# Optimization experiments

Hardware: AMD Instinct MI355X
Metric: run time of the kernel (lower is better)

Reference implementation:

```python
import jax, jax.numpy as jnp
import numpy as np

BIG = 1e8  # sentinel 'infinite' squared distance (sqrt(BIG) >> max real distance)


def _edt_sq(feat):
    """Exact squared Euclidean distance transform to the nearest True pixel.
    feat: (H, W) bool. Separable 1-D min-plus envelopes (exact, matches
    scipy.ndimage.distance_transform_edt with unit sampling)."""
    H, W = feat.shape
    f = jnp.where(feat, 0.0, BIG).astype(jnp.float32)
    iw = jnp.arange(W, dtype=jnp.float32)
    sqw = (iw[:, None] - iw[None, :]) ** 2                      # (Wx, Wy)
    d1 = jnp.min(f[:, None, :] + sqw[None, :, :], axis=-1)      # (H, W) row pass
    ih = jnp.arange(H, dtype=jnp.float32)
    sqh = (ih[:, None] - ih[None, :]) ** 2                      # (Hx, Hy)
    d2 = jnp.min(d1[None, :, :] + sqh[:, :, None], axis=1)      # (H, W) col pass
    return d2


def _phi_one(mask):
    # pos: distance to nearest mask==1 pixel (scipy edt of 1-mask)
    # neg: distance to nearest mask==0 pixel (scipy edt of mask)
    pos = jnp.sqrt(_edt_sq(mask))
    neg = jnp.sqrt(_edt_sq(~mask))
    s = mask.sum()
    return jnp.where(s == 0, pos,
                     jnp.where(s == mask.size, -neg, pos - neg + 1.0))


def _boundary_loss(logits, targets):
    B, C, H, W = logits.shape
    probs = jax.nn.softmax(logits, axis=1)
    # one-hot scatter: (B,H,W) -> (B,C,H,W)
    oh = jax.nn.one_hot(targets, C, dtype=jnp.float32).transpose(0, 3, 1, 2)
    masks = (oh > 0.5).reshape(B * C, H, W)
    phi = jax.lax.map(_phi_one, masks).reshape(B, C, H, W)
    phi = jax.lax.stop_gradient(phi)  # torch computes phi under no_grad
    return jnp.mean(probs * phi)


def setup_inputs() -> dict:
    key = jax.random.key(0)
    k1, k2 = jax.random.split(key)
    B, C, H, W = 8, 4, 384, 384
    logits = jax.random.normal(k1, (B, C, H, W), dtype=jnp.float32)
    targets = jax.random.randint(k2, (B, H, W), 0, C, dtype=jnp.int32)
    return {"logits": logits, "targets": targets}


def reference(logits, targets):
    return _boundary_loss(logits, targets)
```

## Files before the change

kernel.cpp:

```cpp
#include <hip/hip_runtime.h>


#define BB 8
#define CC 4
#define HH 384
#define WW 384
#define HW (HH * WW)
#define EDT16_BYTES ((size_t)BB * CC * HW * 2)
#define NTOT 4718592.0f

__global__ __launch_bounds__(384) void k_rowedt(const int* __restrict__ targets,
                                                unsigned short* __restrict__ edt16,
                                                float* __restrict__ out) {
    const int blk = blockIdx.x;
    const int b = blk / HH;
    const int i = blk - b * HH;
    const int j = threadIdx.x;
    const int wv = j >> 6, ln = j & 63;

    __shared__ unsigned long long msk[CC][6];
    const int tj = targets[((size_t)b * HH + i) * WW + j];

    #pragma unroll
    for (int c = 0; c < CC; ++c) {
        const unsigned long long m = __ballot(tj == c);
        if (ln == 0) msk[c][wv] = m;
    }
    __syncthreads();

    #pragma unroll
    for (int c = 0; c < CC; ++c) {
        const unsigned long long w = msk[c][wv];
        int dR = 0xFFFF;
        const unsigned long long x = (ln == 63) ? 0ull : (w >> (ln + 1));
        if (x) {
            dR = __builtin_ctzll(x) + 1;
        } else {
            for (int k = wv + 1; k < 6; ++k) {
                const unsigned long long wk = msk[c][k];
                if (wk) { dR = 64 * k + __builtin_ctzll(wk) - j; break; }
            }
        }
        int dL = 0xFFFF;
        const unsigned long long y = (ln == 0) ? 0ull : (w << (64 - ln));
        if (y) {
            dL = __builtin_clzll(y) + 1;
        } else {
            for (int k = wv - 1; k >= 0; --k) {
                const unsigned long long wk = msk[c][k];
                if (wk) { dL = j - (64 * k + 63 - __builtin_clzll(wk)); break; }
            }
        }
        const int fd = (tj == c) ? 0 : (dR < dL ? dR : dL);
        edt16[(size_t)(b * CC + c) * HW + (size_t)i * WW + j] = (unsigned short)fd;
    }

    if (blk == 0 && j == 0) out[0] = 0.0f;
}

__global__ __launch_bounds__(384) void k_coledt(const unsigned short* __restrict__ edt16,
                                                float* __restrict__ phi) {
    const int blk = blockIdx.x;
    const int b = blk >> 5;
    const int tile = blk & 31;
    const int j0 = tile * 12;
    const int col = threadIdx.x % 12;
    const int rg  = threadIdx.x / 12;

    __shared__ unsigned short dls[CC][HH][13];

    #pragma unroll
    for (int c = 0; c < CC; ++c) {
        #pragma unroll
        for (int k = 0; k < 12; ++k) {
            const int i = rg * 12 + k;
            dls[c][i][col] =
                edt16[(size_t)(b * CC + c) * HW + (size_t)i * WW + j0 + col];
        }
    }
    __syncthreads();

    #pragma unroll 1
    for (int k = 0; k < 12; ++k) {
        const int i = rg * 12 + k;
        float r4[CC];
        #pragma unroll
        for (int c = 0; c < CC; ++c) {
            const unsigned int v0 = dls[c][i][col];
            float best = (float)(v0 * v0);
            float dd = 1.0f, odd = 3.0f;
            int lo = i, hi = i;
            while (dd < best) {
                lo = (lo > 0) ? lo - 1 : 0;
                hi = (hi < HH - 1) ? hi + 1 : HH - 1;
                const unsigned int a = dls[c][lo][col];
                const unsigned int e = dls[c][hi][col];
                const float ca = (float)(a * a) + dd;
                const float cb = (float)(e * e) + dd;
                best = fminf(best, fminf(ca, cb));
                dd += odd; odd += 2.0f;
            }
            r4[c] = sqrtf(best);
        }
        const float n0 = fminf(r4[1], fminf(r4[2], r4[3]));
        const float n1 = fminf(r4[0], fminf(r4[2], r4[3]));
        const float n2 = fminf(r4[0], fminf(r4[1], r4[3]));
        const float n3 = fminf(r4[0], fminf(r4[1], r4[2]));
        const size_t po = (size_t)i * WW + j0 + col;
        const size_t pb = (size_t)b * CC * HW;
        phi[pb + 0 * HW + po] = r4[0] - n0 + 1.0f;
        phi[pb + 1 * HW + po] = r4[1] - n1 + 1.0f;
        phi[pb + 2 * HW + po] = r4[2] - n2 + 1.0f;
        phi[pb + 3 * HW + po] = r4[3] - n3 + 1.0f;
    }
}

__global__ __launch_bounds__(256) void k_loss(const float* __restrict__ logits,
                                              const float* __restrict__ phi,
                                              float* __restrict__ out) {
    const int tid = blockIdx.x * 256 + threadIdx.x;
    const int b = tid / (HW / 4);
    const int p4 = tid - b * (HW / 4);
    const size_t base = (size_t)b * CC * HW + (size_t)p4 * 4;

    float l[CC][4], ph[CC][4];
    #pragma unroll
    for (int c = 0; c < CC; ++c) {
        const float4 lv = *(const float4*)(logits + base + (size_t)c * HW);
        const float4 pv = *(const float4*)(phi    + base + (size_t)c * HW);
        l[c][0] = lv.x; l[c][1] = lv.y; l[c][2] = lv.z; l[c][3] = lv.w;
        ph[c][0] = pv.x; ph[c][1] = pv.y; ph[c][2] = pv.z; ph[c][3] = pv.w;
    }

    float acc = 0.0f;
    #pragma unroll
    for (int e = 0; e < 4; ++e) {
        const float m = fmaxf(fmaxf(l[0][e], l[1][e]), fmaxf(l[2][e], l[3][e]));
        const float e0 = __expf(l[0][e] - m), e1 = __expf(l[1][e] - m);
        const float e2 = __expf(l[2][e] - m), e3 = __expf(l[3][e] - m);
        const float inv = 1.0f / (e0 + e1 + e2 + e3);
        acc += inv * (e0 * ph[0][e] + e1 * ph[1][e] + e2 * ph[2][e] + e3 * ph[3][e]);
    }

    #pragma unroll
    for (int off = 32; off > 0; off >>= 1) acc += __shfl_down(acc, off, 64);
    __shared__ float wsum[4];
    const int wid = threadIdx.x >> 6, ln = threadIdx.x & 63;
    if (ln == 0) wsum[wid] = acc;
    __syncthreads();
    if (threadIdx.x == 0) {
        atomicAdd(out, (wsum[0] + wsum[1] + wsum[2] + wsum[3]) * (1.0f / NTOT));
    }
}

extern "C" void kernel_launch(void* const* d_in, const int* in_sizes, int n_in,
                              void* d_out, int out_size, void* d_ws, size_t ws_size,
                              hipStream_t stream) {
    const float* logits  = (const float*)d_in[0];
    const int*   targets = (const int*)d_in[1];
    float* out = (float*)d_out;
    unsigned short* edt16 = (unsigned short*)d_ws;
    float* phi = (float*)((unsigned char*)d_ws + EDT16_BYTES);

    hipLaunchKernelGGL(k_rowedt, dim3(BB * HH), dim3(WW), 0, stream, targets, edt16, out);
    hipLaunchKernelGGL(k_coledt, dim3(BB * 32), dim3(384), 0, stream, edt16, phi);
    hipLaunchKernelGGL(k_loss,   dim3(BB * HW / 4 / 256), dim3(256), 0, stream,
                       logits, phi, out);
}
```

Measured before the change: 119.1 us.

## Fuse column EDT pass with softmax-weighted loss reduction, drop phi buffer

Merges the column distance pass and the loss kernel so phi is consumed in registers instead of being written to and re-read from global memory. The column tile widens from 12 to 16 columns, with rows strided across thread groups, giving 192 blocks instead of 256. Logits are now read as scalar per-thread loads of 16-column segments rather than float4 vectors. Fewer blocks and a heavier per-thread workload may reduce parallelism across the GPU's compute units.

```diff
diff --git a/kernel.cpp b/kernel.cpp
--- a/kernel.cpp
+++ b/kernel.cpp
@@ -6,7 +6,6 @@
 #define HH 384
 #define WW 384
 #define HW (HH * WW)
-#define EDT16_BYTES ((size_t)BB * CC * HW * 2)
 #define NTOT 4718592.0f
 
 __global__ __launch_bounds__(384) void k_rowedt(const int* __restrict__ targets,
@@ -58,31 +57,33 @@
     if (blk == 0 && j == 0) out[0] = 0.0f;
 }
 
-__global__ __launch_bounds__(384) void k_coledt(const unsigned short* __restrict__ edt16,
-                                                float* __restrict__ phi) {
+__global__ __launch_bounds__(384) void k_fused(const unsigned short* __restrict__ edt16,
+                                               const float* __restrict__ logits,
+                                               float* __restrict__ out) {
     const int blk = blockIdx.x;
-    const int b = blk >> 5;
-    const int tile = blk & 31;
-    const int j0 = tile * 12;
-    const int col = threadIdx.x % 12;
-    const int rg  = threadIdx.x / 12;
+    const int b = blk / 24;
+    const int tile = blk - b * 24;
+    const int j0 = tile * 16;
+    const int col = threadIdx.x & 15;
+    const int rg  = threadIdx.x >> 4;
 
-    __shared__ unsigned short dls[CC][HH][13];
+    __shared__ unsigned short dls[CC][HH][17];
 
     #pragma unroll
     for (int c = 0; c < CC; ++c) {
         #pragma unroll
-        for (int k = 0; k < 12; ++k) {
-            const int i = rg * 12 + k;
+        for (int k = 0; k < 16; ++k) {
+            const int i = rg + 24 * k;
             dls[c][i][col] =
                 edt16[(size_t)(b * CC + c) * HW + (size_t)i * WW + j0 + col];
         }
     }
     __syncthreads();
 
+    float acc = 0.0f;
     #pragma unroll 1
-    for (int k = 0; k < 12; ++k) {
-        const int i = rg * 12 + k;
+    for (int k = 0; k < 16; ++k) {
+        const int i = rg + 24 * k;
         float r4[CC];
         #pragma unroll
         for (int c = 0; c < CC; ++c) {
@@ -95,61 +96,40 @@
                 hi = (hi < HH - 1) ? hi + 1 : HH - 1;
                 const unsigned int a = dls[c][lo][col];
                 const unsigned int e = dls[c][hi][col];
-                const float ca = (float)(a * a) + dd;
-                const float cb = (float)(e * e) + dd;
-                best = fminf(best, fminf(ca, cb));
+                best = fminf(best, fminf((float)(a * a) + dd, (float)(e * e) + dd));
                 dd += odd; odd += 2.0f;
             }
             r4[c] = sqrtf(best);
         }
-        const float n0 = fminf(r4[1], fminf(r4[2], r4[3]));
-        const float n1 = fminf(r4[0], fminf(r4[2], r4[3]));
-        const float n2 = fminf(r4[0], fminf(r4[1], r4[3]));
-        const float n3 = fminf(r4[0], fminf(r4[1], r4[2]));
+        const float p0 = r4[0] - fminf(r4[1], fminf(r4[2], r4[3])) + 1.0f;
+        const float p1 = r4[1] - fminf(r4[0], fminf(r4[2], r4[3])) + 1.0f;
+        const float p2 = r4[2] - fminf(r4[0], fminf(r4[1], r4[3])) + 1.0f;
+        const float p3 = r4[3] - fminf(r4[0], fminf(r4[1], r4[2])) + 1.0f;
+
         const size_t po = (size_t)i * WW + j0 + col;
         const size_t pb = (size_t)b * CC * HW;
-        phi[pb + 0 * HW + po] = r4[0] - n0 + 1.0f;
-        phi[pb + 1 * HW + po] = r4[1] - n1 + 1.0f;
-        phi[pb + 2 * HW + po] = r4[2] - n2 + 1.0f;
-        phi[pb + 3 * HW + po] = r4[3] - n3 + 1.0f;
-    }
-}
-
-__global__ __launch_bounds__(256) void k_loss(const float* __restrict__ logits,
-                                              const float* __restrict__ phi,
-                                              float* __restrict__ out) {
-    const int tid = blockIdx.x * 256 + threadIdx.x;
-    const int b = tid / (HW / 4);
-    const int p4 = tid - b * (HW / 4);
-    const size_t base = (size_t)b * CC * HW + (size_t)p4 * 4;
-
-    float l[CC][4], ph[CC][4];
-    #pragma unroll
-    for (int c = 0; c < CC; ++c) {
-        const float4 lv = *(const float4*)(logits + base + (size_t)c * HW);
-        const float4 pv = *(const float4*)(phi    + base + (size_t)c * HW);
-        l[c][0] = lv.x; l[c][1] = lv.y; l[c][2] = lv.z; l[c][3] = lv.w;
-        ph[c][0] = pv.x; ph[c][1] = pv.y; ph[c][2] = pv.z; ph[c][3] = pv.w;
-    }
-
-    float acc = 0.0f;
-    #pragma unroll
-    for (int e = 0; e < 4; ++e) {
-        const float m = fmaxf(fmaxf(l[0][e], l[1][e]), fmaxf(l[2][e], l[3][e]));
-        const float e0 = __expf(l[0][e] - m), e1 = __expf(l[1][e] - m);
-        const float e2 = __expf(l[2][e] - m), e3 = __expf(l[3][e] - m);
+        const float l0 = logits[pb + 0 * HW + po];
+        const float l1 = logits[pb + 1 * HW + po];
+        const float l2 = logits[pb + 2 * HW + po];
+        const float l3 = logits[pb + 3 * HW + po];
+        const float m  = fmaxf(fmaxf(l0, l1), fmaxf(l2, l3));
+        const float e0 = __expf(l0 - m), e1 = __expf(l1 - m);
+        const float e2 = __expf(l2 - m), e3 = __expf(l3 - m);
         const float inv = 1.0f / (e0 + e1 + e2 + e3);
-        acc += inv * (e0 * ph[0][e] + e1 * ph[1][e] + e2 * ph[2][e] + e3 * ph[3][e]);
+        acc += inv * (e0 * p0 + e1 * p1 + e2 * p2 + e3 * p3);
     }
 
     #pragma unroll
     for (int off = 32; off > 0; off >>= 1) acc += __shfl_down(acc, off, 64);
-    __shared__ float wsum[4];
+    __shared__ float wsum[6];
     const int wid = threadIdx.x >> 6, ln = threadIdx.x & 63;
     if (ln == 0) wsum[wid] = acc;
     __syncthreads();
     if (threadIdx.x == 0) {
-        atomicAdd(out, (wsum[0] + wsum[1] + wsum[2] + wsum[3]) * (1.0f / NTOT));
+        float tot = 0.0f;
+        #pragma unroll
+        for (int w = 0; w < 6; ++w) tot += wsum[w];
+        atomicAdd(out, tot * (1.0f / NTOT));
     }
 }
 
@@ -160,10 +140,7 @@
     const int*   targets = (const int*)d_in[1];
     float* out = (float*)d_out;
     unsigned short* edt16 = (unsigned short*)d_ws;
-    float* phi = (float*)((unsigned char*)d_ws + EDT16_BYTES);
 
     hipLaunchKernelGGL(k_rowedt, dim3(BB * HH), dim3(WW), 0, stream, targets, edt16, out);
-    hipLaunchKernelGGL(k_coledt, dim3(BB * 32), dim3(384), 0, stream, edt16, phi);
-    hipLaunchKernelGGL(k_loss,   dim3(BB * HW / 4 / 256), dim3(256), 0, stream,
-                       logits, phi, out);
+    hipLaunchKernelGGL(k_fused,  dim3(BB * 24), dim3(384), 0, stream, edt16, logits, out);
 }
```

Result: faster. 103.4 us (-13.2%).
